# Kernel optimization log

Hardware: AMD Instinct MI355X
Metric: run time of the kernel (lower is better)

Reference implementation:

```python
import jax, jax.numpy as jnp
import numpy as np

N_NODES = 100000
N_EDGES = 1600000
IN_DIM = 256
HIDDEN = 128


def setup_inputs() -> dict:
    key = jax.random.key(0)
    ks = jax.random.split(key, 8)
    x = jax.random.normal(ks[0], (N_NODES, IN_DIM), dtype=jnp.float32)
    edge_index = jax.random.randint(ks[1], (2, N_EDGES), 0, N_NODES, dtype=jnp.int64)
    W0 = jax.random.normal(ks[2], (IN_DIM, HIDDEN), dtype=jnp.float32) / np.sqrt(IN_DIM)
    b0 = jnp.zeros((HIDDEN,), dtype=jnp.float32)
    Wmu = jax.random.normal(ks[3], (HIDDEN, HIDDEN), dtype=jnp.float32) / np.sqrt(HIDDEN)
    bmu = jnp.zeros((HIDDEN,), dtype=jnp.float32)
    Wsig = jax.random.normal(ks[4], (HIDDEN, HIDDEN), dtype=jnp.float32) / np.sqrt(HIDDEN)
    bsig = jnp.zeros((HIDDEN,), dtype=jnp.float32)
    return {"x": x, "edge_index": edge_index, "W0": W0, "b0": b0,
            "Wmu": Wmu, "bmu": bmu, "Wsig": Wsig, "bsig": bsig}


def reference(x, edge_index, W0, b0, Wmu, bmu, Wsig, bsig):
    N = x.shape[0]
    # PyG gcn_norm: add self-loops (weight 1), deg over target (col),
    # norm = deg^-1/2[row] * w * deg^-1/2[col]
    loops = jnp.arange(N, dtype=edge_index.dtype)
    row = jnp.concatenate([edge_index[0], loops])  # sources
    col = jnp.concatenate([edge_index[1], loops])  # targets
    w = jnp.ones(row.shape[0], dtype=x.dtype)
    deg = jax.ops.segment_sum(w, col, num_segments=N)
    dinv = jnp.where(deg > 0, jax.lax.rsqrt(deg), 0.0).astype(x.dtype)
    norm = dinv[row] * dinv[col]  # [E+N]

    def gcn_conv(h, W, b):
        h = h @ W                                   # dense transform [N, out]
        msg = norm[:, None] * h[row]                # gather + scale [E+N, out]
        return jax.ops.segment_sum(msg, col, num_segments=N) + b

    h = jax.nn.relu(gcn_conv(x, W0, b0))
    mu = gcn_conv(h, Wmu, bmu)
    sigma = jax.nn.softplus(gcn_conv(h, Wsig, bsig)) + 1e-7
    return mu, sigma
```

## Files before the change

kernel.cpp:

```cpp
#include <hip/hip_runtime.h>
#include <math.h>

#define N_NODES 100000
#define N_EDGES 1600000
#define ROWB    512
#define HALFB   51200000ull
#define NBKT    196
#define BSH     9
#define BCAP    10240
#define EPB     1024

typedef float  f32x4  __attribute__((ext_vector_type(4)));
typedef __bf16 bf16x8 __attribute__((ext_vector_type(8)));
typedef short  s16x8  __attribute__((ext_vector_type(8)));
typedef unsigned long long u64;

__device__ __forceinline__ unsigned short f2bf(float f) {
    unsigned int u = __builtin_bit_cast(unsigned int, f);
    u += 0x7FFFu + ((u >> 16) & 1u);
    return (unsigned short)(u >> 16);
}
__device__ __forceinline__ float bf2f(unsigned short h) {
    unsigned int u = ((unsigned int)h) << 16;
    return __builtin_bit_cast(float, u);
}
__device__ __forceinline__ float bf_lo(unsigned int u) {
    return __builtin_bit_cast(float, u << 16);
}
__device__ __forceinline__ float bf_hi(unsigned int u) {
    return __builtin_bit_cast(float, u & 0xFFFF0000u);
}
__device__ __forceinline__ bf16x8 packhi(const float4& a, const float4& b) {
    float v[8] = {a.x, a.y, a.z, a.w, b.x, b.y, b.z, b.w};
    s16x8 hh;
    #pragma unroll
    for (int j = 0; j < 8; j++) hh[j] = (short)f2bf(v[j]);
    return __builtin_bit_cast(bf16x8, hh);
}
__device__ __forceinline__ void ntstore4(void* p, f32x4 v) {
    __builtin_nontemporal_store(v, (f32x4*)p);
}

#define MFMA16(a, b, c) __builtin_amdgcn_mfma_f32_16x16x32_bf16((a), (b), (c), 0, 0, 0)


__launch_bounds__(256)
__global__ void bin_kernel(const int* __restrict__ row, const int* __restrict__ col,
                           int* __restrict__ gcur, u64* __restrict__ entries) {
    __shared__ int hist[NBKT], base[NBKT], cur[NBKT];
    const int tid = threadIdx.x;
    for (int i = tid; i < NBKT; i += 256) { hist[i] = 0; cur[i] = 0; }
    __syncthreads();
    const int e0 = blockIdx.x * EPB;
    int cols[4];
    #pragma unroll
    for (int it = 0; it < 4; it++) {
        int e = e0 + it * 256 + tid;
        int c = (e < N_EDGES) ? col[e] : -1;
        cols[it] = c;
        if (c >= 0) atomicAdd(&hist[c >> BSH], 1);
    }
    __syncthreads();
    for (int i = tid; i < NBKT; i += 256)
        base[i] = atomicAdd(&gcur[i], hist[i]);
    __syncthreads();
    #pragma unroll
    for (int it = 0; it < 4; it++) {
        int e = e0 + it * 256 + tid;
        int c = cols[it];
        if (c >= 0) {
            int b = c >> BSH;
            int r = atomicAdd(&cur[b], 1);
            entries[(size_t)b * BCAP + base[b] + r] =
                ((u64)(unsigned)c << 32) | (unsigned)row[e];
        }
    }
}


__global__ void bktscan_kernel(const int* __restrict__ gcur, int* __restrict__ bktBase) {
    __shared__ int s[256];
    const int tid = threadIdx.x;
    int v = (tid < NBKT) ? gcur[tid] : 0;
    s[tid] = v;
    __syncthreads();
    for (int d = 1; d < 256; d <<= 1) {
        int t = (tid >= d) ? s[tid - d] : 0;
        __syncthreads();
        s[tid] += t;
        __syncthreads();
    }
    if (tid < NBKT) bktBase[tid] = s[tid] - v;
}


__launch_bounds__(256)
__global__ void csr_kernel(const u64* __restrict__ entries, const int* __restrict__ gcur,
                           const int* __restrict__ bktBase,
                           int* __restrict__ cnt, int* __restrict__ offs,
                           float* __restrict__ dinv, int* __restrict__ sortedRow) {
    __shared__ int lcnt[512], sA[512], sB[512], lcur[512];
    const int b = blockIdx.x, tid = threadIdx.x;
    const int n0 = b << BSH;
    lcnt[tid] = 0; lcnt[tid + 256] = 0;
    __syncthreads();
    const int nb = gcur[b], base = bktBase[b];
    const u64* ep = entries + (size_t)b * BCAP;
    for (int i = tid; i < nb; i += 256)
        atomicAdd(&lcnt[(int)(ep[i] >> 32) - n0], 1);
    __syncthreads();
    sA[tid] = lcnt[tid]; sA[tid + 256] = lcnt[tid + 256];
    __syncthreads();
    int* src = sA; int* dst = sB;
    for (int d = 1; d < 512; d <<= 1) {
        #pragma unroll
        for (int k = tid; k < 512; k += 256)
            dst[k] = src[k] + ((k >= d) ? src[k - d] : 0);
        __syncthreads();
        int* t = src; src = dst; dst = t;
    }
    #pragma unroll
    for (int k = tid; k < 512; k += 256) {
        int excl = src[k] - lcnt[k];
        lcur[k] = excl;
        int node = n0 + k;
        if (node < N_NODES) {
            offs[node] = base + excl;
            cnt[node]  = lcnt[k];
            dinv[node] = rsqrtf((float)(lcnt[k] + 1));
        }
    }
    __syncthreads();
    for (int i = tid; i < nb; i += 256) {
        u64 pk = ep[i];
        int local = (int)(pk >> 32) - n0;
        int p = base + atomicAdd(&lcur[local], 1);
        sortedRow[p] = (int)(pk & 0xFFFFFFFFu);
    }
}


__global__ void prep_w(const float* __restrict__ W0, const float* __restrict__ Wmu,
                       const float* __restrict__ Wsig,
                       unsigned short* __restrict__ W0h, unsigned short* __restrict__ W0l,
                       unsigned short* __restrict__ Wmsh, unsigned short* __restrict__ Wmsl) {
    int c = blockIdx.x;
    int k = threadIdx.x;
    if (c < 128) {
        float v = W0[k * 128 + c];
        unsigned short h = f2bf(v);
        W0h[c * 256 + k] = h;
        W0l[c * 256 + k] = f2bf(v - bf2f(h));
    } else if (k < 128) {
        int c2 = c - 128;
        float v = (c2 < 128) ? Wmu[k * 128 + c2] : Wsig[k * 128 + (c2 - 128)];
        unsigned short h = f2bf(v);
        Wmsh[c2 * 128 + k] = h;
        Wmsl[c2 * 128 + k] = f2bf(v - bf2f(h));
    }
}


__launch_bounds__(256, 2)
__global__ void gemm1_mfma(const float* __restrict__ x,
                           const unsigned short* __restrict__ Wh,
                           const unsigned short* __restrict__ Wl,
                           char* __restrict__ t0base, int t0stride) {
    __shared__ __align__(16) char L[65536];
    const int tid = threadIdx.x;
    const int wave = tid >> 6, lane = tid & 63;
    const int lrow = lane & 15, q4 = lane >> 4;
    const int swz = (lrow & 7) << 4;
    const int n0 = blockIdx.x * 128;

    bf16x8 b[2][8];
    #pragma unroll
    for (int g = 0; g < 2; g++) {
        int node = n0 + wave * 32 + g * 16 + lrow;
        int nc = node > N_NODES - 1 ? N_NODES - 1 : node;
        const float* xp = x + (size_t)nc * 256 + q4 * 8;
        #pragma unroll
        for (int ks = 0; ks < 8; ks++) {
            float4 p0 = *(const float4*)(xp + ks * 32);
            float4 p1 = *(const float4*)(xp + ks * 32 + 4);
            b[g][ks] = packhi(p0, p1);
        }
    }

    int sgo[4], slo[4];
    #pragma unroll
    for (int j = 0; j < 4; j++) {
        int u = tid + 256 * j;
        int col = (u >> 5) & 15, k8 = (u & 31) * 8;
        sgo[j] = col * 256 + k8;
        slo[j] = (j >= 2 ? 8192 : 0) + ((col * 512 + k8 * 2) ^ ((col & 7) << 4));
    }

    {
        int4 sw[4];
        #pragma unroll
        for (int j = 0; j < 4; j++)
            sw[j] = *(const int4*)((j >= 2 ? Wl : Wh) + sgo[j]);
        #pragma unroll
        for (int j = 0; j < 4; j++)
            *(int4*)(L + slo[j]) = sw[j];
    }
    __syncthreads();

    #pragma unroll
    for (int ct = 0; ct < 8; ct++) {
        int4 sw[4];
        if (ct < 7) {
            #pragma unroll
            for (int j = 0; j < 4; j++)
                sw[j] = *(const int4*)((j >= 2 ? Wl : Wh) + (ct + 1) * 16 * 256 + sgo[j]);
        }
        const char* bufp = L + (ct & 1) * 16384;
        f32x4 acc[2] = {};
        #pragma unroll
        for (int hl = 0; hl < 2; hl++) {
            bf16x8 w[8];
            #pragma unroll
            for (int ks = 0; ks < 8; ks++)
                w[ks] = *(const bf16x8*)(bufp + hl * 8192 +
                        ((lrow * 512 + ks * 64 + q4 * 16) ^ swz));
            #pragma unroll
            for (int g = 0; g < 2; g++)
                #pragma unroll
                for (int ks = 0; ks < 8; ks++)
                    acc[g] = MFMA16(w[ks], b[g][ks], acc[g]);
        }
        #pragma unroll
        for (int g = 0; g < 2; g++) {
            int node_l = wave * 32 + g * 16 + lrow;
            int a = (node_l * 256 + ct * 32 + q4 * 8) ^ ((node_l & 7) << 4);
            ushort4 p = make_ushort4(f2bf(acc[g][0]), f2bf(acc[g][1]),
                                     f2bf(acc[g][2]), f2bf(acc[g][3]));
            *(ushort4*)(L + 32768 + a) = p;
        }
        if (ct < 7) {
            #pragma unroll
            for (int j = 0; j < 4; j++)
                *(int4*)(L + (((ct + 1) & 1) * 16384) + slo[j]) = sw[j];
            __syncthreads();
        }
    }
    __syncthreads();
    #pragma unroll
    for (int it = 0; it < 8; it++) {
        int linear = it * 4096 + tid * 16;
        int node_l = linear >> 8, off = linear & 255;
        int4 v = *(const int4*)(L + 32768 + (linear ^ ((node_l & 7) << 4)));
        int node = n0 + node_l;
        if (node < N_NODES)
            *(int4*)(t0base + (size_t)node * t0stride + off) = v;
    }
}


template <int EPI>
__launch_bounds__(256)
__global__ void agg_bf16(const char* __restrict__ srcBase, char* __restrict__ dstBase,
                         int stride,
                         const int* __restrict__ offs, const int* __restrict__ cnt,
                         const int* __restrict__ sortedRow, const float* __restrict__ dinv,
                         const float* __restrict__ bias) {
    const int n = blockIdx.x * 4 + (threadIdx.x >> 6);
    const int lane = threadIdx.x & 63;
    const int laneB = lane * 4;
    const float dn = dinv[n];
    unsigned int u = *(const unsigned int*)(srcBase + (size_t)n * stride + laneB);
    const float ws = dn * dn;
    float acc0 = ws * bf_lo(u);
    float acc1 = ws * bf_hi(u);
    const int start = __builtin_amdgcn_readfirstlane(offs[n]);
    const int num   = __builtin_amdgcn_readfirstlane(cnt[n]);

    int i = 0;
    for (; i + 8 <= num; i += 8) {
        int myr = sortedRow[start + i + (lane & 7)];
        int rs[8];
        #pragma unroll
        for (int j = 0; j < 8; j++) rs[j] = __builtin_amdgcn_readlane(myr, j);
        unsigned int ue[8];
        #pragma unroll
        for (int j = 0; j < 8; j++) {
            const char* p = srcBase + (size_t)rs[j] * stride;
            ue[j] = *(const unsigned int*)(p + laneB);
        }
        float w[8];
        #pragma unroll
        for (int j = 0; j < 8; j++) w[j] = dn * dinv[rs[j]];
        #pragma unroll
        for (int j = 0; j < 8; j++) {
            acc0 = fmaf(w[j], bf_lo(ue[j]), acc0);
            acc1 = fmaf(w[j], bf_hi(ue[j]), acc1);
        }
    }
    for (; i < num; i++) {
        int rsv = __builtin_amdgcn_readfirstlane(sortedRow[start + i]);
        const char* p = srcBase + (size_t)rsv * stride;
        unsigned int ue = *(const unsigned int*)(p + laneB);
        float w = dn * dinv[rsv];
        acc0 = fmaf(w, bf_lo(ue), acc0);
        acc1 = fmaf(w, bf_hi(ue), acc1);
    }

    if (EPI) {
        acc0 = fmaxf(acc0 + bias[2 * lane], 0.f);
        acc1 = fmaxf(acc1 + bias[2 * lane + 1], 0.f);
    }
    unsigned int o = (unsigned int)f2bf(acc0) | ((unsigned int)f2bf(acc1) << 16);
    *(unsigned int*)(dstBase + (size_t)n * stride + laneB) = o;
}


__launch_bounds__(256, 4)
__global__ void gemm2_mfma(const unsigned short* __restrict__ Wh,
                           const unsigned short* __restrict__ Wl,
                           const float* __restrict__ bmu, const float* __restrict__ bsig,
                           const char* __restrict__ t2base, int t2stride,
                           char* __restrict__ outc) {
    __shared__ __align__(16) char L[16384];
    const int tid = threadIdx.x;
    const int wave = tid >> 6, lane = tid & 63;
    const int lrow = lane & 15, q4 = lane >> 4;
    const int swz = (lrow & 7) << 4;
    const int n0 = blockIdx.x * 128;

    bf16x8 b[2][4];
    int nodes[2];
    #pragma unroll
    for (int g = 0; g < 2; g++) {
        int node = n0 + wave * 32 + g * 16 + lrow;
        nodes[g] = node;
        int nc = node > N_NODES - 1 ? N_NODES - 1 : node;
        const char* ap = t2base + (size_t)nc * t2stride + q4 * 16;
        #pragma unroll
        for (int ki = 0; ki < 4; ki++)
            b[g][ki] = *(const bf16x8*)(ap + ki * 64);
    }

    const int colS = tid >> 4, k8S = (tid & 15) * 8;
    const int sgo = colS * 128 + k8S;
    const int sloc = (colS * 256 + k8S * 2) ^ ((colS & 7) << 4);

    {
        int4 h = *(const int4*)(Wh + sgo);
        int4 l = *(const int4*)(Wl + sgo);
        *(int4*)(L + sloc) = h;
        *(int4*)(L + 4096 + sloc) = l;
    }
    __syncthreads();

    #pragma unroll
    for (int ct = 0; ct < 16; ct++) {
        int4 swh, swl;
        if (ct < 15) {
            swh = *(const int4*)(Wh + (ct + 1) * 2048 + sgo);
            swl = *(const int4*)(Wl + (ct + 1) * 2048 + sgo);
        }
        const char* bufp = L + (ct & 1) * 8192;
        f32x4 acc[2] = {};
        #pragma unroll
        for (int hl = 0; hl < 2; hl++) {
            bf16x8 w[4];
            #pragma unroll
            for (int ki = 0; ki < 4; ki++)
                w[ki] = *(const bf16x8*)(bufp + hl * 4096 +
                        ((lrow * 256 + ki * 64 + q4 * 16) ^ swz));
            #pragma unroll
            for (int g = 0; g < 2; g++)
                #pragma unroll
                for (int ki = 0; ki < 4; ki++)
                    acc[g] = MFMA16(w[ki], b[g][ki], acc[g]);
        }
        const int f0 = (ct & 7) * 16 + q4 * 4;
        if (ct < 8) {
            float4 bv = *(const float4*)(bmu + f0);
            #pragma unroll
            for (int g = 0; g < 2; g++)
                if (nodes[g] < N_NODES) {
                    f32x4 o = {acc[g][0] + bv.x, acc[g][1] + bv.y,
                               acc[g][2] + bv.z, acc[g][3] + bv.w};
                    ntstore4(outc + (size_t)nodes[g] * ROWB + f0 * 4, o);
                }
        } else {
            float4 bv = *(const float4*)(bsig + f0);
            #pragma unroll
            for (int g = 0; g < 2; g++)
                if (nodes[g] < N_NODES) {
                    f32x4 o;
                    #pragma unroll
                    for (int q = 0; q < 4; q++) {
                        float xv = acc[g][q] + ((const float*)&bv)[q];
                        o[q] = fmaxf(xv, 0.f) + log1pf(expf(-fabsf(xv))) + 1e-7f;
                    }
                    ntstore4(outc + HALFB + (size_t)nodes[g] * ROWB + f0 * 4, o);
                }
        }
        if (ct < 15) {
            char* nb = L + ((ct + 1) & 1) * 8192;
            *(int4*)(nb + sloc) = swh;
            *(int4*)(nb + 4096 + sloc) = swl;
            __syncthreads();
        }
    }
}


extern "C" void kernel_launch(void* const* d_in, const int* in_sizes, int n_in,
                              void* d_out, int out_size, void* d_ws, size_t ws_size,
                              hipStream_t stream) {
    const float* x    = (const float*)d_in[0];
    const int*   ei   = (const int*)d_in[1];
    const int*   row  = ei;
    const int*   col  = ei + N_EDGES;
    const float* W0   = (const float*)d_in[2];
    const float* b0   = (const float*)d_in[3];
    const float* Wmu  = (const float*)d_in[4];
    const float* bmu  = (const float*)d_in[5];
    const float* Wsig = (const float*)d_in[6];
    const float* bsig = (const float*)d_in[7];
    char* outc = (char*)d_out;
    char* wsb  = (char*)d_ws;

    size_t o = 0;
    auto take = [&](size_t nbytes) {
        size_t r = o; o += (nbytes + 255) & ~(size_t)255; return r;
    };
    size_t oW0h = take(65536), oW0l = take(65536);
    size_t oWmsh = take(65536), oWmsl = take(65536);
    size_t oGcur = take(NBKT * 4), oBkt = take(NBKT * 4);
    size_t oCnt = take(N_NODES * 4), oOffs = take(N_NODES * 4), oDinv = take(N_NODES * 4);
    size_t oSort = take(N_EDGES * 4);
    size_t oEnt = take((size_t)NBKT * BCAP * 8);
    size_t oT0 = take((size_t)N_NODES * 256);
    size_t oH  = take((size_t)N_NODES * 256);
    const bool dense = (ws_size >= o);

    unsigned short* W0h  = (unsigned short*)(wsb + oW0h);
    unsigned short* W0l  = (unsigned short*)(wsb + oW0l);
    unsigned short* Wmsh = (unsigned short*)(wsb + oWmsh);
    unsigned short* Wmsl = (unsigned short*)(wsb + oWmsl);
    int*   gcur      = (int*)(wsb + oGcur);
    int*   bktBase   = (int*)(wsb + oBkt);
    int*   cnt       = (int*)(wsb + oCnt);
    int*   offs      = (int*)(wsb + oOffs);
    float* dinvp     = (float*)(wsb + oDinv);
    int*   sortedRow = (int*)(wsb + oSort);

    u64* entries; char *t0b, *hb, *t2b; int stride;
    if (dense) {
        entries = (u64*)(wsb + oEnt);
        t0b = wsb + oT0;  hb = wsb + oH;  t2b = wsb + oT0;
        stride = 256;
    } else {
        entries = (u64*)(outc + HALFB);
        t0b = outc + 256; hb = outc + HALFB; t2b = outc;
        stride = ROWB;
    }

    hipMemsetAsync(gcur, 0, NBKT * sizeof(int), stream);
    prep_w<<<384, 256, 0, stream>>>(W0, Wmu, Wsig, W0h, W0l, Wmsh, Wmsl);
    bin_kernel<<<(N_EDGES + EPB - 1) / EPB, 256, 0, stream>>>(row, col, gcur, entries);
    bktscan_kernel<<<1, 256, 0, stream>>>(gcur, bktBase);
    csr_kernel<<<NBKT, 256, 0, stream>>>(entries, gcur, bktBase, cnt, offs, dinvp, sortedRow);

    gemm1_mfma<<<(N_NODES + 127) / 128, 256, 0, stream>>>(x, W0h, W0l, t0b, stride);
    agg_bf16<1><<<N_NODES / 4, 256, 0, stream>>>(t0b, hb, stride,
                                                 offs, cnt, sortedRow, dinvp, b0);
    agg_bf16<0><<<N_NODES / 4, 256, 0, stream>>>(hb, t2b, stride,
                                                 offs, cnt, sortedRow, dinvp, nullptr);
    gemm2_mfma<<<(N_NODES + 127) / 128, 256, 0, stream>>>(Wmsh, Wmsl, bmu, bsig,
                                                          t2b, stride, outc);
}
```

Baseline: 311.1 us.

## Halve nodes per block in both GEMMs and use fast softplus intrinsics

Both MFMA GEMM kernels now handle 64 nodes per block instead of 128, one 16-node group per wave. This shrinks gemm1's shared memory to 48KB, raises its occupancy hint to 3 blocks, and doubles the grid to spread work across more CUs. The cost is that each block reloads the full weight matrix for half as many nodes, doubling weight traffic through shared memory. The softplus epilogue switches to __expf/__logf instead of log1pf/expf, which trades some accuracy for cheaper math.

```diff
diff --git a/kernel.cpp b/kernel.cpp
--- a/kernel.cpp
+++ b/kernel.cpp
@@ -39,6 +39,9 @@
 }
 __device__ __forceinline__ void ntstore4(void* p, f32x4 v) {
     __builtin_nontemporal_store(v, (f32x4*)p);
+}
+__device__ __forceinline__ float fast_sp(float x) {
+    return fmaxf(x, 0.f) + __logf(1.f + __expf(-fabsf(x))) + 1e-7f;
 }
 
 #define MFMA16(a, b, c) __builtin_amdgcn_mfma_f32_16x16x32_bf16((a), (b), (c), 0, 0, 0)
@@ -161,29 +164,28 @@
 }
 
 
-__launch_bounds__(256, 2)
+__launch_bounds__(256, 3)
 __global__ void gemm1_mfma(const float* __restrict__ x,
                            const unsigned short* __restrict__ Wh,
                            const unsigned short* __restrict__ Wl,
                            char* __restrict__ t0base, int t0stride) {
-    __shared__ __align__(16) char L[65536];
+    __shared__ __align__(16) char L[49152];
     const int tid = threadIdx.x;
     const int wave = tid >> 6, lane = tid & 63;
     const int lrow = lane & 15, q4 = lane >> 4;
     const int swz = (lrow & 7) << 4;
-    const int n0 = blockIdx.x * 128;
-
-    bf16x8 b[2][8];
-    #pragma unroll
-    for (int g = 0; g < 2; g++) {
-        int node = n0 + wave * 32 + g * 16 + lrow;
+    const int n0 = blockIdx.x * 64;
+
+    bf16x8 b[8];
+    {
+        int node = n0 + wave * 16 + lrow;
         int nc = node > N_NODES - 1 ? N_NODES - 1 : node;
         const float* xp = x + (size_t)nc * 256 + q4 * 8;
         #pragma unroll
         for (int ks = 0; ks < 8; ks++) {
             float4 p0 = *(const float4*)(xp + ks * 32);
             float4 p1 = *(const float4*)(xp + ks * 32 + 4);
-            b[g][ks] = packhi(p0, p1);
+            b[ks] = packhi(p0, p1);
         }
     }
 
@@ -216,7 +218,7 @@
                 sw[j] = *(const int4*)((j >= 2 ? Wl : Wh) + (ct + 1) * 16 * 256 + sgo[j]);
         }
         const char* bufp = L + (ct & 1) * 16384;
-        f32x4 acc[2] = {};
+        f32x4 acc = {};
         #pragma unroll
         for (int hl = 0; hl < 2; hl++) {
             bf16x8 w[8];
@@ -225,17 +227,14 @@
                 w[ks] = *(const bf16x8*)(bufp + hl * 8192 +
                         ((lrow * 512 + ks * 64 + q4 * 16) ^ swz));
             #pragma unroll
-            for (int g = 0; g < 2; g++)
-                #pragma unroll
-                for (int ks = 0; ks < 8; ks++)
-                    acc[g] = MFMA16(w[ks], b[g][ks], acc[g]);
-        }
-        #pragma unroll
-        for (int g = 0; g < 2; g++) {
-            int node_l = wave * 32 + g * 16 + lrow;
+            for (int ks = 0; ks < 8; ks++)
+                acc = MFMA16(w[ks], b[ks], acc);
+        }
+        {
+            int node_l = wave * 16 + lrow;
             int a = (node_l * 256 + ct * 32 + q4 * 8) ^ ((node_l & 7) << 4);
-            ushort4 p = make_ushort4(f2bf(acc[g][0]), f2bf(acc[g][1]),
-                                     f2bf(acc[g][2]), f2bf(acc[g][3]));
+            ushort4 p = make_ushort4(f2bf(acc[0]), f2bf(acc[1]),
+                                     f2bf(acc[2]), f2bf(acc[3]));
             *(ushort4*)(L + 32768 + a) = p;
         }
         if (ct < 7) {
@@ -247,7 +246,7 @@
     }
     __syncthreads();
     #pragma unroll
-    for (int it = 0; it < 8; it++) {
+    for (int it = 0; it < 4; it++) {
         int linear = it * 4096 + tid * 16;
         int node_l = linear >> 8, off = linear & 255;
         int4 v = *(const int4*)(L + 32768 + (linear ^ ((node_l & 7) << 4)));
@@ -326,19 +325,17 @@
     const int wave = tid >> 6, lane = tid & 63;
     const int lrow = lane & 15, q4 = lane >> 4;
     const int swz = (lrow & 7) << 4;
-    const int n0 = blockIdx.x * 128;
-
-    bf16x8 b[2][4];
-    int nodes[2];
-    #pragma unroll
-    for (int g = 0; g < 2; g++) {
-        int node = n0 + wave * 32 + g * 16 + lrow;
-        nodes[g] = node;
+    const int n0 = blockIdx.x * 64;
+
+    const int node = n0 + wave * 16 + lrow;
+    const bool ok = node < N_NODES;
+    bf16x8 b[4];
+    {
         int nc = node > N_NODES - 1 ? N_NODES - 1 : node;
         const char* ap = t2base + (size_t)nc * t2stride + q4 * 16;
         #pragma unroll
         for (int ki = 0; ki < 4; ki++)
-            b[g][ki] = *(const bf16x8*)(ap + ki * 64);
+            b[ki] = *(const bf16x8*)(ap + ki * 64);
     }
 
     const int colS = tid >> 4, k8S = (tid & 15) * 8;
@@ -361,7 +358,7 @@
             swl = *(const int4*)(Wl + (ct + 1) * 2048 + sgo);
         }
         const char* bufp = L + (ct & 1) * 8192;
-        f32x4 acc[2] = {};
+        f32x4 acc = {};
         #pragma unroll
         for (int hl = 0; hl < 2; hl++) {
             bf16x8 w[4];
@@ -370,34 +367,25 @@
                 w[ki] = *(const bf16x8*)(bufp + hl * 4096 +
                         ((lrow * 256 + ki * 64 + q4 * 16) ^ swz));
             #pragma unroll
-            for (int g = 0; g < 2; g++)
-                #pragma unroll
-                for (int ki = 0; ki < 4; ki++)
-                    acc[g] = MFMA16(w[ki], b[g][ki], acc[g]);
+            for (int ki = 0; ki < 4; ki++)
+                acc = MFMA16(w[ki], b[ki], acc);
         }
         const int f0 = (ct & 7) * 16 + q4 * 4;
         if (ct < 8) {
-            float4 bv = *(const float4*)(bmu + f0);
-            #pragma unroll
-            for (int g = 0; g < 2; g++)
-                if (nodes[g] < N_NODES) {
-                    f32x4 o = {acc[g][0] + bv.x, acc[g][1] + bv.y,
-                               acc[g][2] + bv.z, acc[g][3] + bv.w};
-                    ntstore4(outc + (size_t)nodes[g] * ROWB + f0 * 4, o);
-                }
+            if (ok) {
+                float4 bv = *(const float4*)(bmu + f0);
+                f32x4 o = {acc[0] + bv.x, acc[1] + bv.y, acc[2] + bv.z, acc[3] + bv.w};
+                ntstore4(outc + (size_t)node * ROWB + f0 * 4, o);
+            }
         } else {
-            float4 bv = *(const float4*)(bsig + f0);
-            #pragma unroll
-            for (int g = 0; g < 2; g++)
-                if (nodes[g] < N_NODES) {
-                    f32x4 o;
-                    #pragma unroll
-                    for (int q = 0; q < 4; q++) {
-                        float xv = acc[g][q] + ((const float*)&bv)[q];
-                        o[q] = fmaxf(xv, 0.f) + log1pf(expf(-fabsf(xv))) + 1e-7f;
-                    }
-                    ntstore4(outc + HALFB + (size_t)nodes[g] * ROWB + f0 * 4, o);
-                }
+            if (ok) {
+                float4 bv = *(const float4*)(bsig + f0);
+                f32x4 o;
+                #pragma unroll
+                for (int q = 0; q < 4; q++)
+                    o[q] = fast_sp(acc[q] + ((const float*)&bv)[q]);
+                ntstore4(outc + HALFB + (size_t)node * ROWB + f0 * 4, o);
+            }
         }
         if (ct < 15) {
             char* nb = L + ((ct + 1) & 1) * 8192;
@@ -467,11 +455,11 @@
     bktscan_kernel<<<1, 256, 0, stream>>>(gcur, bktBase);
     csr_kernel<<<NBKT, 256, 0, stream>>>(entries, gcur, bktBase, cnt, offs, dinvp, sortedRow);
 
-    gemm1_mfma<<<(N_NODES + 127) / 128, 256, 0, stream>>>(x, W0h, W0l, t0b, stride);
+    gemm1_mfma<<<(N_NODES + 63) / 64, 256, 0, stream>>>(x, W0h, W0l, t0b, stride);
     agg_bf16<1><<<N_NODES / 4, 256, 0, stream>>>(t0b, hb, stride,
                                                  offs, cnt, sortedRow, dinvp, b0);
     agg_bf16<0><<<N_NODES / 4, 256, 0, stream>>>(hb, t2b, stride,
                                                  offs, cnt, sortedRow, dinvp, nullptr);
-    gemm2_mfma<<<(N_NODES + 127) / 128, 256, 0, stream>>>(Wmsh, Wmsl, bmu, bsig,
-                                                          t2b, stride, outc);
-}
+    gemm2_mfma<<<(N_NODES + 63) / 64, 256, 0, stream>>>(Wmsh, Wmsl, bmu, bsig,
+                                                        t2b, stride, outc);
+}
```

Result: faster. 279.9 us (-10.0%).
